# Kernel tuning notes

Hardware: AMD Instinct MI355X
Metric: run time of the kernel (lower is better)

## Reference

```python
import jax, jax.numpy as jnp
import numpy as np

B, L, V, E, H2, M, OOV = 128, 400, 50000, 512, 1024, 1024, 50


def setup_inputs() -> dict:
    key = jax.random.key(0)
    ks = jax.random.split(key, 14)
    s = 0.02
    return {
        "y": jax.random.randint(ks[0], (B,), 0, V),
        "h": jax.random.normal(ks[1], (1, B, H2), jnp.float32),
        "memory_bank": jax.random.normal(ks[2], (B, L, M), jnp.float32),
        "src_mask": jnp.ones((B, L), jnp.float32),
        "max_num_oovs": OOV,
        "src_oov": jax.random.randint(ks[3], (B, L), 0, V + OOV),
        # learned parameters (PyTorch Linear y = x @ W + b with W stored [in, out])
        "emb": jax.random.normal(ks[4], (V, E), jnp.float32) * s,
        "W_ih": jax.random.normal(ks[5], (E, 3 * H2), jnp.float32) * s,   # GRU input weights (r|z|n)
        "W_hh": jax.random.normal(ks[6], (H2, 3 * H2), jnp.float32) * s,  # GRU hidden weights (r|z|n)
        "b_ih": jnp.zeros((3 * H2,), jnp.float32),
        "b_hh": jnp.zeros((3 * H2,), jnp.float32),
        "W_mem": jax.random.normal(ks[7], (M, H2), jnp.float32) * s,      # attention memory_project (no bias)
        "W_dec": jax.random.normal(ks[8], (H2, H2), jnp.float32) * s,     # attention decode_project
        "b_dec": jnp.zeros((H2,), jnp.float32),
        "v": jax.random.normal(ks[9], (H2,), jnp.float32) * s,            # attention score vector (no bias)
        "W_pgen": jax.random.normal(ks[10], (M + H2 + E, 1), jnp.float32) * s,
        "b_pgen": jnp.zeros((1,), jnp.float32),
        "W_v1": jax.random.normal(ks[11], (M + H2, H2), jnp.float32) * s,
        "b_v1": jnp.zeros((H2,), jnp.float32),
        "W_v2": jax.random.normal(ks[12], (H2, V), jnp.float32) * s,
        "b_v2": jnp.zeros((V,), jnp.float32),
    }


def reference(y, h, memory_bank, src_mask, max_num_oovs, src_oov,
              emb, W_ih, W_hh, b_ih, b_hh, W_mem, W_dec, b_dec, v,
              W_pgen, b_pgen, W_v1, b_v1, W_v2, b_v2):
    # --- embedding lookup (single decode step) ---
    y_emb = emb[y]                                    # [B, E]
    h0 = h[-1]                                        # [B, H2]

    # --- one-step GRU (PyTorch gate order r, z, n); dropout is identity (eval) ---
    gi = y_emb @ W_ih + b_ih                          # [B, 3*H2]
    gh = h0 @ W_hh + b_hh
    i_r, i_z, i_n = jnp.split(gi, 3, axis=-1)
    h_r, h_z, h_n = jnp.split(gh, 3, axis=-1)
    r = jax.nn.sigmoid(i_r + h_r)
    z = jax.nn.sigmoid(i_z + h_z)
    n = jnp.tanh(i_n + r * h_n)
    h_next = (1.0 - z) * n + z * h0                   # [B, H2]

    # --- concat (Bahdanau) attention with masked softmax ---
    enc_feat = jnp.einsum('blm,mh->blh', memory_bank, W_mem)   # [B, L, H2]
    dec_feat = h_next @ W_dec + b_dec                           # [B, H2]
    scores = jnp.tanh(enc_feat + dec_feat[:, None, :]) @ v     # [B, L]
    attn = jax.nn.softmax(scores, axis=1) * src_mask
    attn_dist = attn / attn.sum(axis=1, keepdims=True)         # renormalized masked softmax
    context = jnp.einsum('bl,blm->bm', attn_dist, memory_bank) # [B, M]

    # --- vocab distribution ---
    vd_in = jnp.concatenate([context, h_next], axis=1)          # [B, M+H2]
    logits = (vd_in @ W_v1 + b_v1) @ W_v2 + b_v2                # [B, V]
    vocab_dist = jax.nn.softmax(logits, axis=1)

    # --- generation gate ---
    pg_in = jnp.concatenate([context, h_next, y_emb], axis=1)   # [B, M+H2+E]
    p_gen = jax.nn.sigmoid(pg_in @ W_pgen + b_pgen)             # [B, 1]

    # --- copy mechanism: scatter attention mass into extended vocab ---
    vocab_dist_ = p_gen * vocab_dist
    attn_dist_ = (1.0 - p_gen) * attn_dist
    bsz = vocab_dist_.shape[0]
    if max_num_oovs > 0:
        vocab_dist_ = jnp.concatenate(
            [vocab_dist_, jnp.zeros((bsz, max_num_oovs), vocab_dist_.dtype)], axis=1)
    rows = jnp.arange(bsz)[:, None]
    final_dist = vocab_dist_.at[rows, src_oov].add(attn_dist_)  # [B, V+OOV]

    return final_dist, h_next[None], context, attn_dist, p_gen
```

## Files before the change

### kernel.cpp

```cpp
#include <hip/hip_runtime.h>

#define B_   128
#define L_   400
#define V_   50000
#define E_   512
#define H2_  1024
#define M_   1024
#define OOV_ 50
#define VE_  50050
#define BL_  51200

typedef __attribute__((ext_vector_type(8))) short short8;
typedef __attribute__((ext_vector_type(4))) float f32x4;

__device__ __forceinline__ unsigned short f2bf(float f){
  unsigned int u = __builtin_bit_cast(unsigned int, f);
  u = (u + 0x7FFFu + ((u >> 16) & 1u)) >> 16;
  return (unsigned short)u;
}
__device__ __forceinline__ float bf2f(unsigned short s){
  unsigned int u = ((unsigned int)s) << 16;
  return __builtin_bit_cast(float, u);
}

__device__ __forceinline__ void gl_lds16(const void* g, void* l){
  __builtin_amdgcn_global_load_lds(
      (const __attribute__((address_space(1))) unsigned int*)g,
      (__attribute__((address_space(3))) unsigned int*)l, 16, 0, 0);
}

__device__ __forceinline__ float wredsum(float v){
  #pragma unroll
  for (int o = 32; o > 0; o >>= 1) v += __shfl_xor(v, o);
  return v;
}
__device__ __forceinline__ float wredmax(float v){
  #pragma unroll
  for (int o = 32; o > 0; o >>= 1) v = fmaxf(v, __shfl_xor(v, o));
  return v;
}

__device__ __forceinline__ void mb_convert_unit(const float* __restrict__ mb,
                                                unsigned char* __restrict__ mbT, int u){
  int gr  = u >> 7;
  int m16 = u & 127;
  const float* src = mb + (size_t)gr * 1024 + m16 * 8;
  float4 f0 = *(const float4*)src;
  float4 f1 = *(const float4*)(src + 4);
  uint4 w;
  w.x = (unsigned)f2bf(f0.x) | ((unsigned)f2bf(f0.y) << 16);
  w.y = (unsigned)f2bf(f0.z) | ((unsigned)f2bf(f0.w) << 16);
  w.z = (unsigned)f2bf(f1.x) | ((unsigned)f2bf(f1.y) << 16);
  w.w = (unsigned)f2bf(f1.z) | ((unsigned)f2bf(f1.w) << 16);
  int panel = gr >> 7, r = gr & 127;
  int ks = m16 >> 3, c16 = m16 & 7;
  size_t dst = (size_t)panel * 262144 + (size_t)ks * 16384
             + (size_t)((r * 128 + c16 * 16) ^ ((r & 7) << 4));
  *(uint4*)(mbT + dst) = w;
}

__global__ void pre_kernel(const float* __restrict__ mb, unsigned char* __restrict__ mbT,
                           const float* __restrict__ Wm, unsigned char* __restrict__ WTt,
                           const int* __restrict__ y, const float* __restrict__ emb,
                           float* __restrict__ yemb, float* __restrict__ zeroA,
                           float* __restrict__ ctx)
{
  __shared__ float tile[32][33];
  int bid = blockIdx.x, t = threadIdx.x;
  if (bid < 6400){
    mb_convert_unit(mb, mbT, bid * 256 + t);
  } else if (bid < 7424){
    int b2 = bid - 6400;
    int n0 = (b2 & 31) * 32, k0 = (b2 >> 5) * 32;
    int tx = t & 31, ty = t >> 5;
    #pragma unroll
    for (int i = 0; i < 32; i += 8) tile[ty + i][tx] = Wm[(size_t)(k0 + ty + i) * H2_ + n0 + tx];
    __syncthreads();
    if (t < 128){
      int nn = t & 31, k16 = t >> 5;
      int col = n0 + nn, kb = k0 + k16 * 8;
      uint4 w;
      w.x = (unsigned)f2bf(tile[k16*8+0][nn]) | ((unsigned)f2bf(tile[k16*8+1][nn]) << 16);
      w.y = (unsigned)f2bf(tile[k16*8+2][nn]) | ((unsigned)f2bf(tile[k16*8+3][nn]) << 16);
      w.z = (unsigned)f2bf(tile[k16*8+4][nn]) | ((unsigned)f2bf(tile[k16*8+5][nn]) << 16);
      w.w = (unsigned)f2bf(tile[k16*8+6][nn]) | ((unsigned)f2bf(tile[k16*8+7][nn]) << 16);
      int cpn = col >> 7, r = col & 127;
      int ks = kb >> 6, c16 = (kb & 63) >> 3;
      size_t dst = (size_t)cpn * 262144 + (size_t)ks * 16384
                 + (size_t)((r * 128 + c16 * 16) ^ ((r & 7) << 4));
      *(uint4*)(WTt + dst) = w;
    }
  } else if (bid < 7488){
    int idx = (bid - 7424) * 256 + t;
    int b  = idx >> 7;
    int c4 = (idx & 127) << 2;
    float4 v = *(const float4*)(emb + (size_t)y[b] * E_ + c4);
    *(float4*)(yemb + (size_t)b * E_ + c4) = v;
  } else if (bid < 8434){
    int u = (bid - 7488) * 256 + t;
    float4 z = {0.f, 0.f, 0.f, 0.f};
    *(float4*)(zeroA + (size_t)u * 4) = z;
  } else {
    int u = (bid - 8434) * 256 + t;
    float4 z = {0.f, 0.f, 0.f, 0.f};
    *(float4*)(ctx + (size_t)u * 4) = z;
  }
}

__device__ __forceinline__ void gemm128_body(int bx, int by,
                               const float* __restrict__ A, int lda,
                               const float* __restrict__ W, int ldw,
                               const float* __restrict__ bias,
                               float* __restrict__ C, int ldc,
                               int N, int kChunk, int addBias)
{
  int tid = threadIdx.x;
  int wv = tid >> 6, lane = tid & 63, lr = lane & 15, lhi = lane >> 4;
  int colBase = bx * 128 + wv * 32;
  int colL[2];
  colL[0] = min(colBase + lr, N - 1);
  colL[1] = min(colBase + 16 + lr, N - 1);
  int k0 = by * kChunk;

  f32x4 zero = {0.f, 0.f, 0.f, 0.f};
  f32x4 acc[8][2];
  #pragma unroll
  for (int r = 0; r < 8; r++){ acc[r][0] = zero; acc[r][1] = zero; }

  int nks = kChunk >> 5;
  for (int ks = 0; ks < nks; ++ks){
    int k = k0 + ks * 32 + lhi * 8;
    short8 bf[2];
    #pragma unroll
    for (int cf = 0; cf < 2; cf++){
      #pragma unroll
      for (int j = 0; j < 8; j++)
        bf[cf][j] = (short)f2bf(W[(size_t)(k + j) * ldw + colL[cf]]);
    }
    #pragma unroll
    for (int rf = 0; rf < 8; rf++){
      const float* ap = A + (size_t)(rf * 16 + lr) * lda + k;
      float4 a0 = *(const float4*)ap;
      float4 a1 = *(const float4*)(ap + 4);
      short8 af;
      af[0]=(short)f2bf(a0.x); af[1]=(short)f2bf(a0.y); af[2]=(short)f2bf(a0.z); af[3]=(short)f2bf(a0.w);
      af[4]=(short)f2bf(a1.x); af[5]=(short)f2bf(a1.y); af[6]=(short)f2bf(a1.z); af[7]=(short)f2bf(a1.w);
      acc[rf][0] = __builtin_amdgcn_mfma_f32_16x16x32_bf16(af, bf[0], acc[rf][0], 0, 0, 0);
      acc[rf][1] = __builtin_amdgcn_mfma_f32_16x16x32_bf16(af, bf[1], acc[rf][1], 0, 0, 0);
    }
  }

  bool addB = addBias && (by == 0);
  #pragma unroll
  for (int cf = 0; cf < 2; cf++){
    int col = colBase + cf * 16 + lr;
    bool ok = col < N;
    float bv = addB ? bias[colL[cf]] : 0.f;
    #pragma unroll
    for (int rf = 0; rf < 8; rf++)
      #pragma unroll
      for (int i = 0; i < 4; i++){
        int row = rf * 16 + lhi * 4 + i;
        if (ok) atomicAdd(&C[(size_t)row * ldc + col], acc[rf][cf][i] + bv);
      }
  }
}

__launch_bounds__(256)
__global__ void gigh_kernel(const float* __restrict__ yemb, const float* __restrict__ hin,
                            const float* __restrict__ W_ih, const float* __restrict__ W_hh,
                            float* __restrict__ gi, float* __restrict__ gh,
                            const float* __restrict__ mb, unsigned char* __restrict__ mbT){
  int bid = blockIdx.x;
  if (bid < 48)
    gemm128_body(bid % 24, bid / 24, yemb, E_,  W_ih, 3 * H2_, nullptr, gi, 3 * H2_, 3 * H2_, 256, 0);
  else if (bid < 144){
    int b2 = bid - 48;
    gemm128_body(b2 % 24, b2 / 24, hin, H2_, W_hh, 3 * H2_, nullptr, gh, 3 * H2_, 3 * H2_, 256, 0);
  } else {
    mb_convert_unit(mb, mbT, (6400 + bid - 144) * 256 + threadIdx.x);
  }
}

__global__ void gru_gates_kernel(const float* __restrict__ gi, const float* __restrict__ gh,
                                 const float* __restrict__ bih, const float* __restrict__ bhh,
                                 const float* __restrict__ h0, float* __restrict__ hn,
                                 const float* __restrict__ mb, unsigned char* __restrict__ mbT){
  int bid = blockIdx.x;
  if (bid >= 512){
    mb_convert_unit(mb, mbT, (12800 + bid - 512) * 256 + threadIdx.x);
    return;
  }
  int idx = bid * 256 + threadIdx.x;
  int b = idx >> 10, j = idx & 1023;
  const float* gib = gi + (size_t)b * 3072;
  const float* ghb = gh + (size_t)b * 3072;
  float ir = gib[j]        + bih[j],        hr = ghb[j]        + bhh[j];
  float iz = gib[j + 1024] + bih[j + 1024], hz = ghb[j + 1024] + bhh[j + 1024];
  float in_= gib[j + 2048] + bih[j + 2048], hnv= ghb[j + 2048] + bhh[j + 2048];
  float r = 1.f / (1.f + __expf(-(ir + hr)));
  float z = 1.f / (1.f + __expf(-(iz + hz)));
  float n = tanhf(in_ + r * hnv);
  hn[idx] = (1.f - z) * n + z * h0[idx];
}

__launch_bounds__(256)
__global__ void dec_kernel(const float* __restrict__ hnext, const float* __restrict__ W_dec,
                           const float* __restrict__ b_dec, float* __restrict__ dec,
                           const float* __restrict__ mb, unsigned char* __restrict__ mbT){
  int bid = blockIdx.x;
  if (bid < 32)
    gemm128_body(bid & 7, bid >> 3, hnext, H2_, W_dec, H2_, b_dec, dec, H2_, H2_, 256, 1);
  else
    mb_convert_unit(mb, mbT, (19200 + bid - 32) * 256 + threadIdx.x);
}

__launch_bounds__(256)
__global__ void scores_kernel(const unsigned char* __restrict__ mbT,
                              const unsigned char* __restrict__ WTt,
                              const float* __restrict__ dec, const float* __restrict__ vvec,
                              float* __restrict__ scr)
{
  __shared__ __align__(16) unsigned char LDSm[65536];
  const int tid = threadIdx.x, lane = tid & 63;
  const int wv = tid >> 6, lr = lane & 15, lhi = lane >> 4;
  const int wru = wv >> 1, wcu = wv & 1;

  int p = blockIdx.x;
  int lid = (p & 7) * 400 + (p >> 3);
  int rp = lid >> 3, cp = lid & 7;
  int r0 = rp << 7;

  int wvu = __builtin_amdgcn_readfirstlane(wv);
  const unsigned char* segA = mbT + (size_t)rp * 262144 + wvu * 4096 + lane * 16;
  const unsigned char* segB = WTt + (size_t)cp * 262144 + wvu * 4096 + lane * 16;
  const int ldsA = wvu * 4096;
  const int ldsB = 16384 + wvu * 4096;

  int aoff[4], boff[4];
  #pragma unroll
  for (int rf = 0; rf < 4; rf++){
    int row = wru * 64 + rf * 16 + lr;
    aoff[rf] = (row * 128 + lhi * 16) ^ ((row & 7) << 4);
  }
  #pragma unroll
  for (int cf = 0; cf < 4; cf++){
    int col = wcu * 64 + cf * 16 + lr;
    boff[cf] = ((col * 128 + lhi * 16) ^ ((col & 7) << 4)) + 16384;
  }

  f32x4 zero = {0.f, 0.f, 0.f, 0.f};
  f32x4 acc[4][4];
  #pragma unroll
  for (int rf = 0; rf < 4; rf++)
    #pragma unroll
    for (int cf = 0; cf < 4; cf++) acc[rf][cf] = zero;

  #pragma unroll
  for (int j = 0; j < 4; j++){
    gl_lds16(segA + j * 1024, &LDSm[ldsA + j * 1024]);
    gl_lds16(segB + j * 1024, &LDSm[ldsB + j * 1024]);
  }

  #pragma unroll 1
  for (int t = 0; t < 16; ++t){
    const int cur = (t & 1) << 15;
    if (t < 15){
      const size_t soff = (size_t)(t + 1) * 16384;
      const int nb = ((t + 1) & 1) << 15;
      #pragma unroll
      for (int j = 0; j < 4; j++){
        gl_lds16(segA + soff + j * 1024, &LDSm[nb + ldsA + j * 1024]);
        gl_lds16(segB + soff + j * 1024, &LDSm[nb + ldsB + j * 1024]);
      }
      asm volatile("s_waitcnt vmcnt(8)" ::: "memory");
    } else {
      asm volatile("s_waitcnt vmcnt(0)" ::: "memory");
    }
    __builtin_amdgcn_s_barrier();
    __builtin_amdgcn_sched_barrier(0);

    #pragma unroll
    for (int k2 = 0; k2 < 2; k2++){
      short8 af[4], bfr[4];
      #pragma unroll
      for (int rf = 0; rf < 4; rf++) af[rf]  = *(const short8*)&LDSm[cur + (aoff[rf] ^ (k2 << 6))];
      #pragma unroll
      for (int cf = 0; cf < 4; cf++) bfr[cf] = *(const short8*)&LDSm[cur + (boff[cf] ^ (k2 << 6))];
      #pragma unroll
      for (int rf = 0; rf < 4; rf++)
        #pragma unroll
        for (int cf = 0; cf < 4; cf++)
          acc[rf][cf] = __builtin_amdgcn_mfma_f32_16x16x32_bf16(af[rf], bfr[cf], acc[rf][cf], 0, 0, 0);
    }

    __builtin_amdgcn_sched_barrier(0);
    __builtin_amdgcn_s_barrier();
    __builtin_amdgcn_sched_barrier(0);
  }

  int colb = (cp << 7) + wcu * 64 + lr;
  float vv0 = vvec[colb], vv1 = vvec[colb + 16], vv2 = vvec[colb + 32], vv3 = vvec[colb + 48];
  #pragma unroll
  for (int rf = 0; rf < 4; rf++){
    #pragma unroll
    for (int i = 0; i < 4; i++){
      int grow = r0 + wru * 64 + rf * 16 + lhi * 4 + i;
      int bb = grow / 400;
      const float* dp = dec + (size_t)bb * 1024 + colb;
      float x0 = acc[rf][0][i] + dp[0];
      float x1 = acc[rf][1][i] + dp[16];
      float x2 = acc[rf][2][i] + dp[32];
      float x3 = acc[rf][3][i] + dp[48];
      float part = (1.f - 2.f / (__expf(2.f * x0) + 1.f)) * vv0
                 + (1.f - 2.f / (__expf(2.f * x1) + 1.f)) * vv1
                 + (1.f - 2.f / (__expf(2.f * x2) + 1.f)) * vv2
                 + (1.f - 2.f / (__expf(2.f * x3) + 1.f)) * vv3;
      part += __shfl_xor(part, 1);
      part += __shfl_xor(part, 2);
      part += __shfl_xor(part, 4);
      part += __shfl_xor(part, 8);
      if (lr == 0) atomicAdd(&scr[grow], part);
    }
  }
}

__launch_bounds__(256)
__global__ void context_kernel(const float* __restrict__ scr, const float* __restrict__ mask,
                               const unsigned char* __restrict__ mbT,
                               float* __restrict__ ctx, float* __restrict__ attn){
  int b = blockIdx.y, lc = blockIdx.x, t = threadIdx.x;
  int wv = t >> 6, lane = t & 63;
  __shared__ float red[4];
  __shared__ float a[400];
  float s0 = scr[b * 400 + t];
  float s1 = (t < 144) ? scr[b * 400 + t + 256] : -1e30f;
  float m = wredmax(fmaxf(s0, s1));
  if (lane == 0) red[wv] = m;
  __syncthreads();
  float M = fmaxf(fmaxf(red[0], red[1]), fmaxf(red[2], red[3]));
  __syncthreads();
  float e0 = __expf(s0 - M) * mask[b * 400 + t];
  float e1 = (t < 144) ? __expf(s1 - M) * mask[b * 400 + t + 256] : 0.f;
  float s = wredsum(e0 + e1);
  if (lane == 0) red[wv] = s;
  __syncthreads();
  float inv = 1.f / (red[0] + red[1] + red[2] + red[3]);
  a[t] = e0 * inv;
  if (t < 144) a[t + 256] = e1 * inv;
  __syncthreads();
  if (t < 100) attn[b * 400 + lc * 100 + t] = a[lc * 100 + t];

  int u = t & 127;
  int half = t >> 7;
  int ks = u >> 3, c16 = u & 7;
  float sa[8];
  #pragma unroll
  for (int j = 0; j < 8; j++) sa[j] = 0.f;
  for (int l = half; l < 100; l += 2){
    int gr = b * 400 + lc * 100 + l;
    int panel = gr >> 7, r = gr & 127;
    const unsigned char* pp = mbT + (size_t)panel * 262144 + (size_t)ks * 16384
                              + (size_t)((r * 128 + c16 * 16) ^ ((r & 7) << 4));
    short8 v = *(const short8*)pp;
    float al = a[lc * 100 + l];
    #pragma unroll
    for (int j = 0; j < 8; j++) sa[j] += al * bf2f((unsigned short)v[j]);
  }
  float* cp = ctx + (size_t)b * M_ + u * 8;
  #pragma unroll
  for (int j = 0; j < 8; j++) atomicAdd(cp + j, sa[j]);
}

__launch_bounds__(256)
__global__ void v1_pgen_kernel(const float* __restrict__ ctx, const float* __restrict__ hn,
                               const float* __restrict__ yemb,
                               const float* __restrict__ Wv1, const float* __restrict__ bv1,
                               float* __restrict__ vp,
                               const float* __restrict__ Wp, const float* __restrict__ bp,
                               float* __restrict__ pg)
{
  int bid = blockIdx.x;
  if (bid < 64){
    int bx = bid & 7, by = bid >> 3;
    int tid = threadIdx.x;
    int wv = tid >> 6, lane = tid & 63, lr = lane & 15, lhi = lane >> 4;
    int colBase = bx * 128 + wv * 32;
    const float* Asrc = (by < 4) ? ctx : hn;
    int k0 = ((by < 4) ? by : (by - 4)) * 256;
    int wk0 = by * 256;

    f32x4 zero = {0.f, 0.f, 0.f, 0.f};
    f32x4 acc[8][2];
    #pragma unroll
    for (int r = 0; r < 8; r++){ acc[r][0] = zero; acc[r][1] = zero; }

    for (int ks = 0; ks < 8; ++ks){
      int k  = k0 + ks * 32 + lhi * 8;
      int wk = wk0 + ks * 32 + lhi * 8;
      short8 bf[2];
      #pragma unroll
      for (int cf = 0; cf < 2; cf++){
        #pragma unroll
        for (int j = 0; j < 8; j++)
          bf[cf][j] = (short)f2bf(Wv1[(size_t)(wk + j) * H2_ + colBase + cf * 16 + lr]);
      }
      #pragma unroll
      for (int rf = 0; rf < 8; rf++){
        const float* ap = Asrc + (size_t)(rf * 16 + lr) * 1024 + k;
        float4 a0 = *(const float4*)ap;
        float4 a1 = *(const float4*)(ap + 4);
        short8 af;
        af[0]=(short)f2bf(a0.x); af[1]=(short)f2bf(a0.y); af[2]=(short)f2bf(a0.z); af[3]=(short)f2bf(a0.w);
        af[4]=(short)f2bf(a1.x); af[5]=(short)f2bf(a1.y); af[6]=(short)f2bf(a1.z); af[7]=(short)f2bf(a1.w);
        acc[rf][0] = __builtin_amdgcn_mfma_f32_16x16x32_bf16(af, bf[0], acc[rf][0], 0, 0, 0);
        acc[rf][1] = __builtin_amdgcn_mfma_f32_16x16x32_bf16(af, bf[1], acc[rf][1], 0, 0, 0);
      }
    }

    float* Cw = vp + (size_t)by * 131072;
    bool addB = (by == 0);
    #pragma unroll
    for (int cf = 0; cf < 2; cf++){
      int col = colBase + cf * 16 + lr;
      float bv = addB ? bv1[col] : 0.f;
      #pragma unroll
      for (int rf = 0; rf < 8; rf++)
        #pragma unroll
        for (int i = 0; i < 4; i++){
          int row = rf * 16 + lhi * 4 + i;
          Cw[(size_t)row * H2_ + col] = acc[rf][cf][i] + bv;
        }
    }
  } else {
    int b = bid - 64, t = threadIdx.x, wv = t >> 6, lane = t & 63;
    __shared__ float red[4];
    float s = 0.f;
    for (int i = t; i < 1024; i += 256) s += ctx[(size_t)b * 1024 + i] * Wp[i];
    for (int i = t; i < 1024; i += 256) s += hn[(size_t)b * 1024 + i] * Wp[1024 + i];
    for (int i = t; i < 512;  i += 256) s += yemb[(size_t)b * 512 + i] * Wp[2048 + i];
    s = wredsum(s);
    if (lane == 0) red[wv] = s;
    __syncthreads();
    if (t == 0){
      float S = red[0] + red[1] + red[2] + red[3] + bp[0];
      pg[b] = 1.f / (1.f + __expf(-S));
    }
  }
}

__global__ void hid2bf_kernel(const float* __restrict__ vp, unsigned short* __restrict__ hb){
  int id = blockIdx.x * 256 + threadIdx.x;
  float4 s = *(const float4*)(vp + (size_t)id * 4);
  #pragma unroll
  for (int ky = 1; ky < 8; ky++){
    float4 v = *(const float4*)(vp + (size_t)ky * 131072 + (size_t)id * 4);
    s.x += v.x; s.y += v.y; s.z += v.z; s.w += v.w;
  }
  ushort2 p0 = {f2bf(s.x), f2bf(s.y)};
  ushort2 p1 = {f2bf(s.z), f2bf(s.w)};
  *(ushort2*)(hb + (size_t)id * 4)     = p0;
  *(ushort2*)(hb + (size_t)id * 4 + 2) = p1;
}

__launch_bounds__(256)
__global__ void gemm_bfA_kernel(const unsigned short* __restrict__ A,
                                const float* __restrict__ W,
                                const float* __restrict__ bias,
                                float* __restrict__ C, int N)
{
  int tid = threadIdx.x;
  int wv = tid >> 6, lane = tid & 63, lr = lane & 15, lhi = lane >> 4;
  int colBase = blockIdx.x * 128 + wv * 32;
  int colL[2];
  colL[0] = min(colBase + lr, N - 1);
  colL[1] = min(colBase + 16 + lr, N - 1);

  f32x4 zero = {0.f, 0.f, 0.f, 0.f};
  f32x4 acc[8][2];
  #pragma unroll
  for (int r = 0; r < 8; r++){ acc[r][0] = zero; acc[r][1] = zero; }

  for (int ks = 0; ks < 32; ++ks){
    int k = ks * 32 + lhi * 8;
    short8 bf[2];
    #pragma unroll
    for (int cf = 0; cf < 2; cf++){
      #pragma unroll
      for (int j = 0; j < 8; j++)
        bf[cf][j] = (short)f2bf(W[(size_t)(k + j) * N + colL[cf]]);
    }
    #pragma unroll
    for (int rf = 0; rf < 8; rf++){
      short8 af = *(const short8*)(A + (size_t)(rf * 16 + lr) * 1024 + k);
      acc[rf][0] = __builtin_amdgcn_mfma_f32_16x16x32_bf16(af, bf[0], acc[rf][0], 0, 0, 0);
      acc[rf][1] = __builtin_amdgcn_mfma_f32_16x16x32_bf16(af, bf[1], acc[rf][1], 0, 0, 0);
    }
  }

  #pragma unroll
  for (int cf = 0; cf < 2; cf++){
    int col = colBase + cf * 16 + lr;
    bool ok = col < N;
    float bv = bias[colL[cf]];
    #pragma unroll
    for (int rf = 0; rf < 8; rf++)
      #pragma unroll
      for (int i = 0; i < 4; i++){
        int row = rf * 16 + lhi * 4 + i;
        if (ok) C[(size_t)row * V_ + col] = acc[rf][cf][i] + bv;
      }
  }
}

__global__ void vocab_softmax_kernel(const float* __restrict__ lg0, const float* __restrict__ pg,
                                     const float* __restrict__ attn, const int* __restrict__ soov,
                                     float* __restrict__ fin){
  int b = blockIdx.x, t = threadIdx.x, wv = t >> 6, lane = t & 63;
  __shared__ float redm[16], reds[16];
  const float* l0 = lg0 + (size_t)b * V_;
  float m = -1e30f, s = 0.f;
  for (int i = t; i < V_; i += 1024){
    float l = l0[i];
    float mn = fmaxf(m, l);
    s = s * __expf(m - mn) + __expf(l - mn);
    m = mn;
  }
  #pragma unroll
  for (int o = 32; o > 0; o >>= 1){
    float mo = __shfl_xor(m, o), so = __shfl_xor(s, o);
    float mn = fmaxf(m, mo);
    s = s * __expf(m - mn) + so * __expf(mo - mn);
    m = mn;
  }
  if (lane == 0){ redm[wv] = m; reds[wv] = s; }
  __syncthreads();
  float M = -1e30f;
  #pragma unroll
  for (int w = 0; w < 16; w++) M = fmaxf(M, redm[w]);
  float S = 0.f;
  #pragma unroll
  for (int w = 0; w < 16; w++) S += reds[w] * __expf(redm[w] - M);
  float pgb = pg[b];
  float scale = pgb / S;
  float* fb = fin + (size_t)b * VE_;
  for (int i = t; i < V_; i += 1024) fb[i] = __expf(l0[i] - M) * scale;
  for (int i = V_ + t; i < VE_; i += 1024) fb[i] = 0.f;
  __syncthreads();
  float om = 1.f - pgb;
  if (t < 400) atomicAdd(&fb[soov[b * 400 + t]], om * attn[b * 400 + t]);
}

extern "C" void kernel_launch(void* const* d_in, const int* in_sizes, int n_in,
                              void* d_out, int out_size, void* d_ws, size_t ws_size,
                              hipStream_t stream)
{
  const int*   y     = (const int*)  d_in[0];
  const float* hin   = (const float*)d_in[1];
  const float* mb    = (const float*)d_in[2];
  const float* mask  = (const float*)d_in[3];
  const int*   soov  = (const int*)  d_in[5];
  const float* emb   = (const float*)d_in[6];
  const float* W_ih  = (const float*)d_in[7];
  const float* W_hh  = (const float*)d_in[8];
  const float* b_ih  = (const float*)d_in[9];
  const float* b_hh  = (const float*)d_in[10];
  const float* W_mem = (const float*)d_in[11];
  const float* W_dec = (const float*)d_in[12];
  const float* b_dec = (const float*)d_in[13];
  const float* vvec  = (const float*)d_in[14];
  const float* W_pg  = (const float*)d_in[15];
  const float* b_pg  = (const float*)d_in[16];
  const float* W_v1  = (const float*)d_in[17];
  const float* b_v1  = (const float*)d_in[18];
  const float* W_v2  = (const float*)d_in[19];
  const float* b_v2  = (const float*)d_in[20];

  float* out   = (float*)d_out;
  float* fin   = out;
  float* hnext = out + (size_t)B_ * VE_;
  float* ctx   = hnext + (size_t)B_ * H2_;
  float* attn  = ctx + (size_t)B_ * M_;
  float* pg    = attn + (size_t)B_ * L_;

  float* ws   = (float*)d_ws;
  float* yemb = ws;
  float* gi   = ws + 65536;
  float* gh   = gi + 393216;
  float* dec  = gh + 393216;
  float* scr  = dec + 131072;
  float* lg0  = scr + 51200;
  float* vp   = lg0;
  unsigned short* hidbf = (unsigned short*)(lg0 + 6400000);
  unsigned char*  WTt   = (unsigned char*)(hidbf + 131072);
  unsigned char*  mbT   = WTt + 2097152;

  pre_kernel<<<8562, 256, 0, stream>>>(mb, mbT, W_mem, WTt, y, emb, yemb, gi, ctx);
  gigh_kernel<<<6544, 256, 0, stream>>>(yemb, hin, W_ih, W_hh, gi, gh, mb, mbT);
  gru_gates_kernel<<<6912, 256, 0, stream>>>(gi, gh, b_ih, b_hh, hin, hnext, mb, mbT);
  dec_kernel<<<6432, 256, 0, stream>>>(hnext, W_dec, b_dec, dec, mb, mbT);

  scores_kernel<<<3200, 256, 0, stream>>>(mbT, WTt, dec, vvec, scr);
  context_kernel<<<dim3(4, 128), 256, 0, stream>>>(scr, mask, mbT, ctx, attn);

  v1_pgen_kernel<<<192, 256, 0, stream>>>(ctx, hnext, yemb, W_v1, b_v1, vp, W_pg, b_pg, pg);
  hid2bf_kernel<<<128, 256, 0, stream>>>(vp, hidbf);
  gemm_bfA_kernel<<<391, 256, 0, stream>>>(hidbf, W_v2, b_v2, lg0, V_);

  vocab_softmax_kernel<<<128, 1024, 0, stream>>>(lg0, pg, attn, soov, fin);
}
```

Before: 504.1 us.

## Pre-convert W_v2 to bf16 in scores kernel and replace score atomics with partials

New measurement: 542.8 us. +7.7%, slower.

```diff
diff --git a/kernel.cpp b/kernel.cpp
--- a/kernel.cpp
+++ b/kernel.cpp
@@ -21,6 +21,9 @@
 __device__ __forceinline__ float bf2f(unsigned short s){
   unsigned int u = ((unsigned int)s) << 16;
   return __builtin_bit_cast(float, u);
+}
+__device__ __forceinline__ short f2bf_t(float f){
+  return (short)(__builtin_bit_cast(unsigned int, f) >> 16);
 }
 
 __device__ __forceinline__ void gl_lds16(const void* g, void* l){
@@ -96,12 +99,12 @@
     int c4 = (idx & 127) << 2;
     float4 v = *(const float4*)(emb + (size_t)y[b] * E_ + c4);
     *(float4*)(yemb + (size_t)b * E_ + c4) = v;
-  } else if (bid < 8434){
+  } else if (bid < 8384){
     int u = (bid - 7488) * 256 + t;
     float4 z = {0.f, 0.f, 0.f, 0.f};
     *(float4*)(zeroA + (size_t)u * 4) = z;
   } else {
-    int u = (bid - 8434) * 256 + t;
+    int u = (bid - 8384) * 256 + t;
     float4 z = {0.f, 0.f, 0.f, 0.f};
     *(float4*)(ctx + (size_t)u * 4) = z;
   }
@@ -219,14 +222,29 @@
 __global__ void scores_kernel(const unsigned char* __restrict__ mbT,
                               const unsigned char* __restrict__ WTt,
                               const float* __restrict__ dec, const float* __restrict__ vvec,
-                              float* __restrict__ scr)
+                              float* __restrict__ scrp,
+                              const float* __restrict__ Wv2, unsigned short* __restrict__ wv2bf)
 {
   __shared__ __align__(16) unsigned char LDSm[65536];
   const int tid = threadIdx.x, lane = tid & 63;
+  int p = blockIdx.x;
+
+  if (p >= 3200){
+    int u = (p - 3200) * 256 + tid;
+    const float4* s = (const float4*)(Wv2 + (size_t)u * 8);
+    float4 f0 = s[0], f1 = s[1];
+    uint4 w;
+    w.x = (unsigned)f2bf(f0.x) | ((unsigned)f2bf(f0.y) << 16);
+    w.y = (unsigned)f2bf(f0.z) | ((unsigned)f2bf(f0.w) << 16);
+    w.z = (unsigned)f2bf(f1.x) | ((unsigned)f2bf(f1.y) << 16);
+    w.w = (unsigned)f2bf(f1.z) | ((unsigned)f2bf(f1.w) << 16);
+    *(uint4*)(wv2bf + (size_t)u * 8) = w;
+    return;
+  }
+
   const int wv = tid >> 6, lr = lane & 15, lhi = lane >> 4;
   const int wru = wv >> 1, wcu = wv & 1;
 
-  int p = blockIdx.x;
   int lid = (p & 7) * 400 + (p >> 3);
   int rp = lid >> 3, cp = lid & 7;
   int r0 = rp << 7;
@@ -320,21 +338,32 @@
       part += __shfl_xor(part, 2);
       part += __shfl_xor(part, 4);
       part += __shfl_xor(part, 8);
-      if (lr == 0) atomicAdd(&scr[grow], part);
+      if (lr == 0) scrp[(size_t)grow * 16 + cp * 2 + wcu] = part;
     }
   }
 }
 
 __launch_bounds__(256)
-__global__ void context_kernel(const float* __restrict__ scr, const float* __restrict__ mask,
+__global__ void context_kernel(const float* __restrict__ scrp, const float* __restrict__ mask,
                                const unsigned char* __restrict__ mbT,
                                float* __restrict__ ctx, float* __restrict__ attn){
   int b = blockIdx.y, lc = blockIdx.x, t = threadIdx.x;
   int wv = t >> 6, lane = t & 63;
   __shared__ float red[4];
   __shared__ float a[400];
-  float s0 = scr[b * 400 + t];
-  float s1 = (t < 144) ? scr[b * 400 + t + 256] : -1e30f;
+  int row0 = b * 400 + t;
+  float s0 = 0.f, s1;
+  {
+    const float4* p0 = (const float4*)(scrp + (size_t)row0 * 16);
+    #pragma unroll
+    for (int q = 0; q < 4; q++){ float4 v = p0[q]; s0 += v.x + v.y + v.z + v.w; }
+    if (t < 144){
+      s1 = 0.f;
+      const float4* p1 = (const float4*)(scrp + (size_t)(row0 + 256) * 16);
+      #pragma unroll
+      for (int q = 0; q < 4; q++){ float4 v = p1[q]; s1 += v.x + v.y + v.z + v.w; }
+    } else s1 = -1e30f;
+  }
   float m = wredmax(fmaxf(s0, s1));
   if (lane == 0) red[wv] = m;
   __syncthreads();
@@ -488,7 +517,57 @@
     for (int cf = 0; cf < 2; cf++){
       #pragma unroll
       for (int j = 0; j < 8; j++)
-        bf[cf][j] = (short)f2bf(W[(size_t)(k + j) * N + colL[cf]]);
+        bf[cf][j] = f2bf_t(W[(size_t)(k + j) * N + colL[cf]]);
+    }
+    #pragma unroll
+    for (int rf = 0; rf < 8; rf++){
+      short8 af = *(const short8*)(A + (size_t)(rf * 16 + lr) * 1024 + k);
+      acc[rf][0] = __builtin_amdgcn_mfma_f32_16x16x32_bf16(af, bf[0], acc[rf][0], 0, 0, 0);
+      acc[rf][1] = __builtin_amdgcn_mfma_f32_16x16x32_bf16(af, bf[1], acc[rf][1], 0, 0, 0);
+    }
+  }
+
+  #pragma unroll
+  for (int cf = 0; cf < 2; cf++){
+    int col = colBase + cf * 16 + lr;
+    bool ok = col < N;
+    float bv = bias[colL[cf]];
+    #pragma unroll
+    for (int rf = 0; rf < 8; rf++)
+      #pragma unroll
+      for (int i = 0; i < 4; i++){
+        int row = rf * 16 + lhi * 4 + i;
+        if (ok) C[(size_t)row * V_ + col] = acc[rf][cf][i] + bv;
+      }
+  }
+}
+
+__launch_bounds__(256)
+__global__ void gemm_bfA_bfW_kernel(const unsigned short* __restrict__ A,
+                                    const unsigned short* __restrict__ Wb,
+                                    const float* __restrict__ bias,
+                                    float* __restrict__ C, int N)
+{
+  int tid = threadIdx.x;
+  int wv = tid >> 6, lane = tid & 63, lr = lane & 15, lhi = lane >> 4;
+  int colBase = blockIdx.x * 128 + wv * 32;
+  int colL[2];
+  colL[0] = min(colBase + lr, N - 1);
+  colL[1] = min(colBase + 16 + lr, N - 1);
+
+  f32x4 zero = {0.f, 0.f, 0.f, 0.f};
+  f32x4 acc[8][2];
+  #pragma unroll
+  for (int r = 0; r < 8; r++){ acc[r][0] = zero; acc[r][1] = zero; }
+
+  for (int ks = 0; ks < 32; ++ks){
+    int k = ks * 32 + lhi * 8;
+    short8 bf[2];
+    #pragma unroll
+    for (int cf = 0; cf < 2; cf++){
+      #pragma unroll
+      for (int j = 0; j < 8; j++)
+        bf[cf][j] = (short)Wb[(size_t)(k + j) * N + colL[cf]];
     }
     #pragma unroll
     for (int rf = 0; rf < 8; rf++){
@@ -588,24 +667,31 @@
   float* gi   = ws + 65536;
   float* gh   = gi + 393216;
   float* dec  = gh + 393216;
-  float* scr  = dec + 131072;
-  float* lg0  = scr + 51200;
+  float* scrp = dec + 131072;
+  float* lg0  = scrp + 819200;
   float* vp   = lg0;
   unsigned short* hidbf = (unsigned short*)(lg0 + 6400000);
   unsigned char*  WTt   = (unsigned char*)(hidbf + 131072);
   unsigned char*  mbT   = WTt + 2097152;
-
-  pre_kernel<<<8562, 256, 0, stream>>>(mb, mbT, W_mem, WTt, y, emb, yemb, gi, ctx);
+  unsigned short* wv2bf = (unsigned short*)(mbT + 104857600);
+
+  const bool useBfW = ws_size >= (size_t)242425856;
+  const int scoresGrid = useBfW ? (3200 + 25000) : 3200;
+
+  pre_kernel<<<8512, 256, 0, stream>>>(mb, mbT, W_mem, WTt, y, emb, yemb, gi, ctx);
   gigh_kernel<<<6544, 256, 0, stream>>>(yemb, hin, W_ih, W_hh, gi, gh, mb, mbT);
   gru_gates_kernel<<<6912, 256, 0, stream>>>(gi, gh, b_ih, b_hh, hin, hnext, mb, mbT);
   dec_kernel<<<6432, 256, 0, stream>>>(hnext, W_dec, b_dec, dec, mb, mbT);
 
-  scores_kernel<<<3200, 256, 0, stream>>>(mbT, WTt, dec, vvec, scr);
-  context_kernel<<<dim3(4, 128), 256, 0, stream>>>(scr, mask, mbT, ctx, attn);
+  scores_kernel<<<scoresGrid, 256, 0, stream>>>(mbT, WTt, dec, vvec, scrp, W_v2, wv2bf);
+  context_kernel<<<dim3(4, 128), 256, 0, stream>>>(scrp, mask, mbT, ctx, attn);
 
   v1_pgen_kernel<<<192, 256, 0, stream>>>(ctx, hnext, yemb, W_v1, b_v1, vp, W_pg, b_pg, pg);
   hid2bf_kernel<<<128, 256, 0, stream>>>(vp, hidbf);
-  gemm_bfA_kernel<<<391, 256, 0, stream>>>(hidbf, W_v2, b_v2, lg0, V_);
+  if (useBfW)
+    gemm_bfA_bfW_kernel<<<391, 256, 0, stream>>>(hidbf, wv2bf, b_v2, lg0, V_);
+  else
+    gemm_bfA_kernel<<<391, 256, 0, stream>>>(hidbf, W_v2, b_v2, lg0, V_);
 
   vocab_softmax_kernel<<<128, 1024, 0, stream>>>(lg0, pg, attn, soov, fin);
 }
```
